# Kernel optimization log

Hardware: AMD Instinct MI355X
Metric: run time of the kernel (lower is better)

## Reference

```python
import jax, jax.numpy as jnp
import numpy as np

D_MODEL = 1024
EXPAND = 2
D_INNER = D_MODEL * EXPAND  # 2048
D_STATE = 16
FFN_HIDDEN = ((D_MODEL * 4 * 2 // 3) + 63) // 64 * 64  # 2752
EPS = 1e-6


def rmsnorm(x, w):
    return x * jax.lax.rsqrt(jnp.mean(x * x, axis=-1, keepdims=True) + EPS) * w


def selective_scan(z, dt_w, dt_b, x_proj_w, A_log, Dp):
    # z: [B, L, d_inner]
    dt = jax.nn.softplus(jnp.einsum('bld,ed->ble', z, dt_w) + dt_b)     # [B,L,d]
    BC = jnp.einsum('bld,nd->bln', z, x_proj_w)                          # [B,L,2n]
    Bm, Cm = BC[..., :D_STATE], BC[..., D_STATE:]                        # [B,L,n]
    A = -jnp.exp(A_log)                                                  # [d,n]
    dA = jnp.exp(dt[..., None] * A)                                      # [B,L,d,n]
    dBz = (dt * z)[..., None] * Bm[:, :, None, :]                        # [B,L,d,n]

    def combine(e1, e2):
        a1, b1 = e1
        a2, b2 = e2
        return (a1 * a2, a2 * b1 + b2)

    _, h = jax.lax.associative_scan(combine, (dA, dBz), axis=1)          # [B,L,d,n]
    y = jnp.einsum('bldn,bln->bld', h, Cm) + z * Dp
    return y


def setup_inputs() -> dict:
    key = jax.random.key(0)
    ks = jax.random.split(key, 12)
    s = 0.02
    inp = {
        'x': jax.random.normal(ks[0], (2, 1024, D_MODEL), dtype=jnp.float32),
        'norm1_w': jnp.ones((D_MODEL,), jnp.float32),
        'in_proj_w': jax.random.normal(ks[1], (D_INNER, D_MODEL), jnp.float32) * s,
        'gate_proj_w': jax.random.normal(ks[2], (D_INNER, D_MODEL), jnp.float32) * s,
        'dt_w': jax.random.normal(ks[3], (D_INNER, D_INNER), jnp.float32) * s,
        'dt_b': jnp.full((D_INNER,), -2.0, jnp.float32),
        'x_proj_w': jax.random.normal(ks[4], (2 * D_STATE, D_INNER), jnp.float32) * s,
        'A_log': jnp.broadcast_to(jnp.log(jnp.arange(1, D_STATE + 1, dtype=jnp.float32)), (D_INNER, D_STATE)).copy(),
        'Dp': jnp.ones((D_INNER,), jnp.float32),
        'out_proj_w': jax.random.normal(ks[5], (D_MODEL, D_INNER), jnp.float32) * s,
        'ffn_norm_w': jnp.ones((D_MODEL,), jnp.float32),
        'ffn_gate_w': jax.random.normal(ks[6], (FFN_HIDDEN, D_MODEL), jnp.float32) * s,
        'ffn_up_w': jax.random.normal(ks[7], (FFN_HIDDEN, D_MODEL), jnp.float32) * s,
        'ffn_down_w': jax.random.normal(ks[8], (D_MODEL, FFN_HIDDEN), jnp.float32) * s,
    }
    return inp


def reference(x, norm1_w, in_proj_w, gate_proj_w, dt_w, dt_b, x_proj_w, A_log, Dp,
              out_proj_w, ffn_norm_w, ffn_gate_w, ffn_up_w, ffn_down_w):
    residual = x
    h = rmsnorm(x, norm1_w)
    z = jnp.einsum('bld,ed->ble', h, in_proj_w)
    gate = jax.nn.sigmoid(jnp.einsum('bld,ed->ble', h, gate_proj_w))
    z = z * gate
    ssm_out = selective_scan(z, dt_w, dt_b, x_proj_w, A_log, Dp)
    x = residual + jnp.einsum('ble,de->bld', ssm_out, out_proj_w)
    hn = rmsnorm(x, ffn_norm_w)
    ff = jnp.einsum('blh,dh->bld',
                    jax.nn.silu(jnp.einsum('bld,hd->blh', hn, ffn_gate_w)) *
                    jnp.einsum('bld,hd->blh', hn, ffn_up_w),
                    ffn_down_w)
    return x + ff
```

## Files before the change

### kernel.cpp

```cpp
#include <hip/hip_runtime.h>
#include <cstdint>
#include <cstddef>


#define BM 128
#define BN 128
#define BK 32

typedef __attribute__((ext_vector_type(8))) short short8;
typedef __attribute__((ext_vector_type(4))) float floatx4;

__device__ __forceinline__ unsigned short f2bf(float f) {
  unsigned int u = __builtin_bit_cast(unsigned int, f);
  u = u + 0x7fffu + ((u >> 16) & 1u);
  return (unsigned short)(u >> 16);
}

__device__ __forceinline__ void async_copy16(const unsigned short* g, unsigned short* l) {
  __builtin_amdgcn_global_load_lds(
      (__attribute__((address_space(1))) void*)(const_cast<unsigned short*>(g)),
      (__attribute__((address_space(3))) void*)(l), 16, 0, 0);
}

struct Seg { const float* src; unsigned short* dst; int mode; int aux; };
struct CvtArgs { Seg sg[10]; int g0[11]; };

__global__ __launch_bounds__(256) void cvt_all(
    CvtArgs a, int nCvt,
    const float* __restrict__ x, const float* __restrict__ nw,
    unsigned short* __restrict__ h_bf) {
  __shared__ float ws_[4];
  if ((int)blockIdx.x >= nCvt) {
    int row = blockIdx.x - nCvt, t = threadIdx.x;
    float4 v = *(const float4*)&x[(size_t)row * 1024 + t * 4];
    float ss = v.x * v.x + v.y * v.y + v.z * v.z + v.w * v.w;
#pragma unroll
    for (int m = 1; m < 64; m <<= 1) ss += __shfl_xor(ss, m);
    if ((t & 63) == 0) ws_[t >> 6] = ss;
    __syncthreads();
    float tot = ws_[0] + ws_[1] + ws_[2] + ws_[3];
    float scale = rsqrtf(tot * (1.0f / 1024.0f) + 1e-6f);
    ushort4 o;
    o.x = f2bf(v.x * scale * nw[t * 4 + 0]);
    o.y = f2bf(v.y * scale * nw[t * 4 + 1]);
    o.z = f2bf(v.z * scale * nw[t * 4 + 2]);
    o.w = f2bf(v.w * scale * nw[t * 4 + 3]);
    *(ushort4*)&h_bf[(size_t)row * 1024 + t * 4] = o;
    return;
  }
  int i = blockIdx.x * 256 + threadIdx.x;
  if (i >= a.g0[10]) return;
  int s = 0;
#pragma unroll
  for (int k = 1; k < 10; ++k) s += (i >= a.g0[k]) ? 1 : 0;
  int li = i - a.g0[s];
  Seg sg = a.sg[s];
  if (sg.mode == 2) {
    ushort4 z = {0, 0, 0, 0};
    *(ushort4*)&sg.dst[(size_t)li * 4] = z;
  } else if (sg.mode == 0) {
    float4 v = *(const float4*)&sg.src[(size_t)li * 4];
    ushort4 o = {f2bf(v.x), f2bf(v.y), f2bf(v.z), f2bf(v.w)};
    *(ushort4*)&sg.dst[(size_t)li * 4] = o;
  } else {
    int r = li >> 8, c = li & 255;
    float4 v = *(const float4*)&sg.src[(size_t)li * 4];
    ushort4 o = {f2bf(v.x), f2bf(v.y), f2bf(v.z), f2bf(v.w)};
    *(ushort4*)&sg.dst[((size_t)(2 * r + sg.aux) * 256 + c) * 4] = o;
  }
}

__global__ __launch_bounds__(256) void rmsnorm_fuse3(
    const float* __restrict__ x, const float* __restrict__ p,
    const float* __restrict__ w,
    float* __restrict__ x2, unsigned short* __restrict__ outbf) {
  int row = blockIdx.x, t = threadIdx.x;
  size_t off = (size_t)row * 1024 + t * 4;
  float4 a = *(const float4*)&x[off];
  float4 b = *(const float4*)&p[off];
  float4 c = *(const float4*)&p[2097152ull + off];
  float4 d = *(const float4*)&p[4194304ull + off];
  float4 e = *(const float4*)&p[6291456ull + off];
  float4 v = {a.x + b.x + c.x + d.x + e.x, a.y + b.y + c.y + d.y + e.y,
              a.z + b.z + c.z + d.z + e.z, a.w + b.w + c.w + d.w + e.w};
  *(float4*)&x2[off] = v;
  float ss = v.x * v.x + v.y * v.y + v.z * v.z + v.w * v.w;
#pragma unroll
  for (int m = 1; m < 64; m <<= 1) ss += __shfl_xor(ss, m);
  __shared__ float ws_[4];
  if ((t & 63) == 0) ws_[t >> 6] = ss;
  __syncthreads();
  float tot = ws_[0] + ws_[1] + ws_[2] + ws_[3];
  float scale = rsqrtf(tot * (1.0f / 1024.0f) + 1e-6f);
  ushort4 o;
  o.x = f2bf(v.x * scale * w[t * 4 + 0]);
  o.y = f2bf(v.y * scale * w[t * 4 + 1]);
  o.z = f2bf(v.z * scale * w[t * 4 + 2]);
  o.w = f2bf(v.w * scale * w[t * 4 + 3]);
  *(ushort4*)&outbf[off] = o;
}

__global__ void final_add(const float* __restrict__ x2, const float* __restrict__ p,
                          float* __restrict__ out) {
  int i = blockIdx.x * 256 + threadIdx.x;
  float4 a = ((const float4*)x2)[i];
  float4 b = ((const float4*)p)[i];
  float4 c = ((const float4*)(p + 2097152ull))[i];
  float4 d = ((const float4*)(p + 4194304ull))[i];
  float4 e = ((const float4*)(p + 6291456ull))[i];
  float4 o = {a.x + b.x + c.x + d.x + e.x, a.y + b.y + c.y + d.y + e.y,
              a.z + b.z + c.z + d.z + e.z, a.w + b.w + c.w + d.w + e.w};
  ((float4*)out)[i] = o;
}

template <int EPI, int MAP>
__global__ __launch_bounds__(256, 4) void gemm_bt(
    const unsigned short* __restrict__ A,
    const unsigned short* __restrict__ W1,
    const unsigned short* __restrict__ W2,
    int n1_blocks, int ncols, int K,
    void* __restrict__ Cv, int ldc,
    float* __restrict__ C2) {
  __shared__ __align__(16) unsigned short As[2][BM * BK];
  __shared__ __align__(16) unsigned short Bs[2][BN * BK];
  int bn, bm, ks = 0, k0 = 0, nk;
  if (MAP == 0) {
    bn = blockIdx.x; bm = blockIdx.y;
    nk = K / BK;
  } else if (MAP == 2) {
    int l = blockIdx.x, i = l >> 3;
    bn = (l & 7) + 8 * (i % 6);
    bm = i / 6;
    if (bn >= ncols) return;
    nk = K / BK;
  } else if (MAP == 3) {
    bn = blockIdx.x & 7; bm = blockIdx.y;
    ks = blockIdx.x >> 3;
    int nkt = K / BK, base = nkt >> 2, rem = nkt & 3;
    nk = base + (ks < rem ? 1 : 0);
    int k0t = ks * base + (ks < rem ? ks : rem);
    k0 = k0t * BK;
  } else {
    if ((int)blockIdx.y < gridDim.y - 1) { bn = blockIdx.x; bm = blockIdx.y; }
    else                                 { bn = n1_blocks;  bm = blockIdx.x; }
    ks = blockIdx.z;
    k0 = ks * (K >> 1);
    nk = (K >> 1) / BK;
  }
  const int tid = threadIdx.x;
  const int wave = tid >> 6, lane = tid & 63;
  const unsigned short* W;
  int wrow0;
  if (bn < n1_blocks) { W = W1; wrow0 = bn * BN; }
  else                { W = W2; wrow0 = (bn - n1_blocks) * BN; }
  const int m0 = bm * BM;
  const int wm = wave >> 1, wn = wave & 1;
  const int l15 = lane & 15, quad = lane >> 4;

  floatx4 acc[4][4] = {};

  const int c0 = wave * 64 + lane;
  const int r0 = c0 >> 2, k0off = ((c0 & 3) ^ ((r0 >> 1) & 3)) * 8;
  const int c1 = c0 + 256;
  const int r1 = c1 >> 2, k1off = ((c1 & 3) ^ ((r1 >> 1) & 3)) * 8;

  auto stage = [&](int kb, int buf) {
    async_copy16(A + (size_t)(m0 + r0) * K + kb + k0off, &As[buf][c0 * 8]);
    async_copy16(A + (size_t)(m0 + r1) * K + kb + k1off, &As[buf][c1 * 8]);
    async_copy16(W + (size_t)(wrow0 + r0) * K + kb + k0off, &Bs[buf][c0 * 8]);
    async_copy16(W + (size_t)(wrow0 + r1) * K + kb + k1off, &Bs[buf][c1 * 8]);
  };

  stage(k0, 0);
  for (int kt = 0; kt < nk; ++kt) {
    const int cur = kt & 1;
    __syncthreads();
    if (kt + 1 < nk) stage(k0 + (kt + 1) * BK, cur ^ 1);

    short8 af[4], bf4[4];
#pragma unroll
    for (int i = 0; i < 4; ++i) {
      int row = wm * 64 + i * 16 + l15;
      af[i] = *(const short8*)&As[cur][(row * 4 + (quad ^ ((row >> 1) & 3))) * 8];
    }
#pragma unroll
    for (int j = 0; j < 4; ++j) {
      int row = wn * 64 + j * 16 + l15;
      bf4[j] = *(const short8*)&Bs[cur][(row * 4 + (quad ^ ((row >> 1) & 3))) * 8];
    }
#pragma unroll
    for (int i = 0; i < 4; ++i)
#pragma unroll
      for (int j = 0; j < 4; ++j)
        acc[i][j] = __builtin_amdgcn_mfma_f32_16x16x32_bf16(af[i], bf4[j], acc[i][j], 0, 0, 0);
  }

#pragma unroll
  for (int i = 0; i < 4; ++i)
#pragma unroll
    for (int j = 0; j < 4; ++j)
#pragma unroll
      for (int r = 0; r < 4; ++r) {
        int gr = m0 + wm * 64 + i * 16 + quad * 4 + r;
        int lc = wn * 64 + j * 16 + l15;
        int gc = bn * BN + lc;
        float v = acc[i][j][r];
        if (EPI == 3) {
          ((float*)Cv)[(size_t)ks * 2097152 + (size_t)gr * ldc + gc] = v;
        } else if (EPI == 4) {
          if (bn < n1_blocks)
            ((float*)Cv)[(size_t)ks * 4194304 + (size_t)gr * ldc + gc] = v;
          else
            C2[(size_t)ks * 262144 + (size_t)gr * 128 + lc] = v;
        } else if (EPI == 5) {
          float other = __shfl_xor(v, 1);
          if (!(l15 & 1)) {
            float zv = v / (1.0f + __expf(-other));
            int f = gc >> 1;
            ((float*)Cv)[(size_t)gr * 2048 + f] = zv;
            ((unsigned short*)C2)[(size_t)gr * 2048 + f] = f2bf(zv);
          }
        } else {
          float other = __shfl_xor(v, 1);
          if (!(l15 & 1)) {
            int f = gc >> 1;
            if (f < 2752) {
              float av = v / (1.0f + __expf(-v)) * other;
              ((unsigned short*)Cv)[(size_t)gr * 2752 + f] = f2bf(av);
            }
          }
        }
      }
}

__device__ __forceinline__ void stage_bc2(const float* __restrict__ pb,
                                          int b, int c, float* bcs, int tid) {
  int row = tid >> 3, c4 = tid & 7;
  size_t idx = ((size_t)b * 1024 + c * 32 + row) * 128 + c4 * 4;
  float4 aa = *(const float4*)&pb[idx];
  float4 bb = *(const float4*)&pb[262144ull + idx];
  float4 sm = {aa.x + bb.x, aa.y + bb.y, aa.z + bb.z, aa.w + bb.w};
  *(float4*)&bcs[row * 32 + c4 * 4] = sm;
}

__device__ __forceinline__ float softplus_f(float v) {
  return fmaxf(v, 0.0f) + log1pf(__expf(-fabsf(v)));
}

__global__ __launch_bounds__(256) void scan_phase1(
    const float* __restrict__ pd, const float* __restrict__ pb,
    const float* __restrict__ dtb, const float* __restrict__ z,
    const float* __restrict__ A_log,
    float* __restrict__ P, float* __restrict__ S) {
  const int d = blockIdx.x * 256 + threadIdx.x;
  const int c = blockIdx.y, b = blockIdx.z;
  __shared__ float bcs[1024];
  stage_bc2(pb, b, c, bcs, threadIdx.x);
  __syncthreads();
  float A2[16];
#pragma unroll
  for (int n = 0; n < 16; ++n) A2[n] = -__expf(A_log[d * 16 + n]) * 1.44269504f;
  const float bias = dtb[d];
  float p[16], s[16];
#pragma unroll
  for (int n = 0; n < 16; ++n) { p[n] = 1.0f; s[n] = 0.0f; }
  const size_t base = ((size_t)b * 1024 + c * 32) * 2048 + d;
#pragma unroll 4
  for (int t = 0; t < 32; ++t) {
    size_t off = base + (size_t)t * 2048;
    float dtv = softplus_f(pd[off] + pd[4194304ull + off] + bias);
    float zv  = z[off];
    float dtz = dtv * zv;
#pragma unroll
    for (int n = 0; n < 16; ++n) {
      float dA = exp2f(dtv * A2[n]);
      s[n] = __builtin_fmaf(dA, s[n], dtz * bcs[t * 32 + n]);
      p[n] *= dA;
    }
  }
  float* Pp = P + (((size_t)c * 2 + b) * 2048 + d) * 16;
  float* Sp = S + (((size_t)c * 2 + b) * 2048 + d) * 16;
#pragma unroll
  for (int n = 0; n < 16; ++n) { Pp[n] = p[n]; Sp[n] = s[n]; }
}

__global__ __launch_bounds__(256) void scan_phase2(
    const float* __restrict__ P, const float* __restrict__ S,
    float* __restrict__ H) {
  int i = blockIdx.x * 256 + threadIdx.x;
  float h = 0.0f;
#pragma unroll
  for (int c = 0; c < 32; ++c) {
    size_t idx = (size_t)c * 65536 + i;
    H[idx] = h;
    h = __builtin_fmaf(P[idx], h, S[idx]);
  }
}

__global__ __launch_bounds__(256) void scan_phase3(
    const float* __restrict__ pd, const float* __restrict__ pb,
    const float* __restrict__ dtb, const float* __restrict__ z,
    const float* __restrict__ A_log, const float* __restrict__ Dp,
    const float* __restrict__ H, unsigned short* __restrict__ ybf) {
  const int d = blockIdx.x * 256 + threadIdx.x;
  const int c = blockIdx.y, b = blockIdx.z;
  __shared__ float bcs[1024];
  stage_bc2(pb, b, c, bcs, threadIdx.x);
  __syncthreads();
  float A2[16];
#pragma unroll
  for (int n = 0; n < 16; ++n) A2[n] = -__expf(A_log[d * 16 + n]) * 1.44269504f;
  const float bias = dtb[d];
  float h[16];
  const float* Hp = H + (((size_t)c * 2 + b) * 2048 + d) * 16;
#pragma unroll
  for (int n = 0; n < 16; ++n) h[n] = Hp[n];
  const float Dd = Dp[d];
  const size_t base = ((size_t)b * 1024 + c * 32) * 2048 + d;
#pragma unroll 4
  for (int t = 0; t < 32; ++t) {
    size_t off = base + (size_t)t * 2048;
    float dtv = softplus_f(pd[off] + pd[4194304ull + off] + bias);
    float zv  = z[off];
    float dtz = dtv * zv;
    float y = zv * Dd;
#pragma unroll
    for (int n = 0; n < 16; ++n) {
      float dA = exp2f(dtv * A2[n]);
      h[n] = __builtin_fmaf(dA, h[n], dtz * bcs[t * 32 + n]);
      y = __builtin_fmaf(h[n], bcs[t * 32 + 16 + n], y);
    }
    ybf[off] = f2bf(y);
  }
}

extern "C" void kernel_launch(void* const* d_in, const int* in_sizes, int n_in,
                              void* d_out, int out_size, void* d_ws, size_t ws_size,
                              hipStream_t stream) {
  const float* x         = (const float*)d_in[0];
  const float* norm1_w   = (const float*)d_in[1];
  const float* in_proj_w = (const float*)d_in[2];
  const float* gate_w    = (const float*)d_in[3];
  const float* dt_w      = (const float*)d_in[4];
  const float* dt_b      = (const float*)d_in[5];
  const float* x_proj_w  = (const float*)d_in[6];
  const float* A_log     = (const float*)d_in[7];
  const float* Dp        = (const float*)d_in[8];
  const float* out_w     = (const float*)d_in[9];
  const float* ffn_nw    = (const float*)d_in[10];
  const float* ffn_g     = (const float*)d_in[11];
  const float* ffn_u     = (const float*)d_in[12];
  const float* ffn_d     = (const float*)d_in[13];
  float* out = (float*)d_out;

  char* p = (char*)d_ws;
  auto alloc = [&](size_t b) { char* r = p; p += (b + 255) & ~(size_t)255; return r; };
  unsigned short* h_bf   = (unsigned short*)alloc(2048ull * 1024 * 2);
  float* big             = (float*)alloc(2048ull * 5632 * 4);
  float* pk              = (float*)alloc(4ull * 2048 * 1024 * 4);
  float* pkb             = (float*)alloc(2ull * 2048 * 128 * 4);
  float* z32             = (float*)alloc(2048ull * 2048 * 4);
  unsigned short* zbf    = (unsigned short*)alloc(2048ull * 2048 * 2);
  unsigned short* ybf    = (unsigned short*)alloc(2048ull * 2048 * 2);
  float* x2              = (float*)alloc(2048ull * 1024 * 4);
  unsigned short* hn_bf  = (unsigned short*)alloc(2048ull * 1024 * 2);
  unsigned short* act_bf = (unsigned short*)alloc(2048ull * 2752 * 2);
  unsigned short* w_zg   = (unsigned short*)alloc(4096ull * 1024 * 2);
  unsigned short* w_dt   = (unsigned short*)alloc(2048ull * 2048 * 2);
  unsigned short* w_xp   = (unsigned short*)alloc(128ull * 2048 * 2);
  unsigned short* w_out  = (unsigned short*)alloc(1024ull * 2048 * 2);
  unsigned short* w_gu   = (unsigned short*)alloc(5632ull * 1024 * 2);
  unsigned short* w_d    = (unsigned short*)alloc(1024ull * 2752 * 2);

  float* pkd = big;
  float* Pb = pk;
  float* Sb = pk + 2097152;
  float* Hb = pk + 4194304;

  CvtArgs ca;
  auto seg = [&](int idx, const float* s, unsigned short* d, int mode, int aux, int groups,
                 int& acc_g) {
    ca.sg[idx] = {s, d, mode, aux};
    ca.g0[idx] = acc_g;
    acc_g += groups;
  };
  int acc_g = 0;
  seg(0, in_proj_w, w_zg,                 1, 0, 2048 * 256, acc_g);
  seg(1, gate_w,    w_zg,                 1, 1, 2048 * 256, acc_g);
  seg(2, dt_w,      w_dt,                 0, 0, 2048 * 512, acc_g);
  seg(3, x_proj_w,  w_xp,                 0, 0, 32 * 512,   acc_g);
  seg(4, nullptr,   w_xp + 32ull * 2048,  2, 0, 96 * 512,   acc_g);
  seg(5, out_w,     w_out,                0, 0, 1024 * 512, acc_g);
  seg(6, ffn_g,     w_gu,                 1, 0, 2752 * 256, acc_g);
  seg(7, ffn_u,     w_gu,                 1, 1, 2752 * 256, acc_g);
  seg(8, nullptr,   w_gu + 5504ull * 1024, 2, 0, 128 * 256, acc_g);
  seg(9, ffn_d,     w_d,                  0, 0, 1024 * 688, acc_g);
  ca.g0[10] = acc_g;
  int nCvt = (acc_g + 255) / 256;
  cvt_all<<<nCvt + 2048, 256, 0, stream>>>(ca, nCvt, x, norm1_w, h_bf);

  gemm_bt<5, 0><<<dim3(32, 16), 256, 0, stream>>>(h_bf, w_zg, w_zg, 32, 0, 1024, z32, 2048, (float*)zbf);
  gemm_bt<4, 4><<<dim3(16, 17, 2), 256, 0, stream>>>(zbf, w_dt, w_xp, 16, 0, 2048, pkd, 2048, pkb);
  scan_phase1<<<dim3(8, 32, 2), 256, 0, stream>>>(pkd, pkb, dt_b, z32, A_log, Pb, Sb);
  scan_phase2<<<256, 256, 0, stream>>>(Pb, Sb, Hb);
  scan_phase3<<<dim3(8, 32, 2), 256, 0, stream>>>(pkd, pkb, dt_b, z32, A_log, Dp, Hb, ybf);
  gemm_bt<3, 3><<<dim3(32, 16), 256, 0, stream>>>(ybf, w_out, w_out, 8, 0, 2048, pk, 1024, nullptr);
  rmsnorm_fuse3<<<2048, 256, 0, stream>>>(x, pk, ffn_nw, x2, hn_bf);
  gemm_bt<6, 2><<<768, 256, 0, stream>>>(hn_bf, w_gu, w_gu, 44, 44, 1024, act_bf, 2752, nullptr);
  gemm_bt<3, 3><<<dim3(32, 16), 256, 0, stream>>>(act_bf, w_d, w_d, 8, 0, 2752, pk, 1024, nullptr);
  final_add<<<2048, 256, 0, stream>>>(x2, pk, out);
}
```

Before: 400.7 us.

## Halve scan chunk length and cache softplus dt between scan phases

The chunked selective scan now uses 64 chunks of 16 timesteps instead of 32 chunks of 32, doubling the number of blocks in phases 1 and 3 so more of the GPU is occupied. Phase 1 also writes the softplus dt values to a new fp32 buffer, and phase 3 reads them back instead of reloading two split-K partials and recomputing softplus. Phase 2's sequential pass becomes twice as long, P/S/H storage doubles (H moves into the big buffer), and the extra dt write/read adds memory traffic.

```diff
diff --git a/kernel.cpp b/kernel.cpp
--- a/kernel.cpp
+++ b/kernel.cpp
@@ -233,14 +233,19 @@
       }
 }
 
+#define NCH 64
+#define CHL 16
+
 __device__ __forceinline__ void stage_bc2(const float* __restrict__ pb,
                                           int b, int c, float* bcs, int tid) {
-  int row = tid >> 3, c4 = tid & 7;
-  size_t idx = ((size_t)b * 1024 + c * 32 + row) * 128 + c4 * 4;
-  float4 aa = *(const float4*)&pb[idx];
-  float4 bb = *(const float4*)&pb[262144ull + idx];
-  float4 sm = {aa.x + bb.x, aa.y + bb.y, aa.z + bb.z, aa.w + bb.w};
-  *(float4*)&bcs[row * 32 + c4 * 4] = sm;
+  if (tid < 128) {
+    int row = tid >> 3, c4 = tid & 7;
+    size_t idx = ((size_t)b * 1024 + c * CHL + row) * 128 + c4 * 4;
+    float4 aa = *(const float4*)&pb[idx];
+    float4 bb = *(const float4*)&pb[262144ull + idx];
+    float4 sm = {aa.x + bb.x, aa.y + bb.y, aa.z + bb.z, aa.w + bb.w};
+    *(float4*)&bcs[row * 32 + c4 * 4] = sm;
+  }
 }
 
 __device__ __forceinline__ float softplus_f(float v) {
@@ -250,11 +255,11 @@
 __global__ __launch_bounds__(256) void scan_phase1(
     const float* __restrict__ pd, const float* __restrict__ pb,
     const float* __restrict__ dtb, const float* __restrict__ z,
-    const float* __restrict__ A_log,
+    const float* __restrict__ A_log, float* __restrict__ dt32,
     float* __restrict__ P, float* __restrict__ S) {
   const int d = blockIdx.x * 256 + threadIdx.x;
   const int c = blockIdx.y, b = blockIdx.z;
-  __shared__ float bcs[1024];
+  __shared__ float bcs[CHL * 32];
   stage_bc2(pb, b, c, bcs, threadIdx.x);
   __syncthreads();
   float A2[16];
@@ -264,11 +269,12 @@
   float p[16], s[16];
 #pragma unroll
   for (int n = 0; n < 16; ++n) { p[n] = 1.0f; s[n] = 0.0f; }
-  const size_t base = ((size_t)b * 1024 + c * 32) * 2048 + d;
+  const size_t base = ((size_t)b * 1024 + c * CHL) * 2048 + d;
 #pragma unroll 4
-  for (int t = 0; t < 32; ++t) {
+  for (int t = 0; t < CHL; ++t) {
     size_t off = base + (size_t)t * 2048;
     float dtv = softplus_f(pd[off] + pd[4194304ull + off] + bias);
+    dt32[off] = dtv;
     float zv  = z[off];
     float dtz = dtv * zv;
 #pragma unroll
@@ -290,7 +296,7 @@
   int i = blockIdx.x * 256 + threadIdx.x;
   float h = 0.0f;
 #pragma unroll
-  for (int c = 0; c < 32; ++c) {
+  for (int c = 0; c < NCH; ++c) {
     size_t idx = (size_t)c * 65536 + i;
     H[idx] = h;
     h = __builtin_fmaf(P[idx], h, S[idx]);
@@ -298,29 +304,28 @@
 }
 
 __global__ __launch_bounds__(256) void scan_phase3(
-    const float* __restrict__ pd, const float* __restrict__ pb,
-    const float* __restrict__ dtb, const float* __restrict__ z,
-    const float* __restrict__ A_log, const float* __restrict__ Dp,
-    const float* __restrict__ H, unsigned short* __restrict__ ybf) {
+    const float* __restrict__ dt32, const float* __restrict__ pb,
+    const float* __restrict__ z, const float* __restrict__ A_log,
+    const float* __restrict__ Dp, const float* __restrict__ H,
+    unsigned short* __restrict__ ybf) {
   const int d = blockIdx.x * 256 + threadIdx.x;
   const int c = blockIdx.y, b = blockIdx.z;
-  __shared__ float bcs[1024];
+  __shared__ float bcs[CHL * 32];
   stage_bc2(pb, b, c, bcs, threadIdx.x);
   __syncthreads();
   float A2[16];
 #pragma unroll
   for (int n = 0; n < 16; ++n) A2[n] = -__expf(A_log[d * 16 + n]) * 1.44269504f;
-  const float bias = dtb[d];
   float h[16];
   const float* Hp = H + (((size_t)c * 2 + b) * 2048 + d) * 16;
 #pragma unroll
   for (int n = 0; n < 16; ++n) h[n] = Hp[n];
   const float Dd = Dp[d];
-  const size_t base = ((size_t)b * 1024 + c * 32) * 2048 + d;
+  const size_t base = ((size_t)b * 1024 + c * CHL) * 2048 + d;
 #pragma unroll 4
-  for (int t = 0; t < 32; ++t) {
+  for (int t = 0; t < CHL; ++t) {
     size_t off = base + (size_t)t * 2048;
-    float dtv = softplus_f(pd[off] + pd[4194304ull + off] + bias);
+    float dtv = dt32[off];
     float zv  = z[off];
     float dtz = dtv * zv;
     float y = zv * Dd;
@@ -361,6 +366,7 @@
   float* pkb             = (float*)alloc(2ull * 2048 * 128 * 4);
   float* z32             = (float*)alloc(2048ull * 2048 * 4);
   unsigned short* zbf    = (unsigned short*)alloc(2048ull * 2048 * 2);
+  float* dt32            = (float*)alloc(2048ull * 2048 * 4);
   unsigned short* ybf    = (unsigned short*)alloc(2048ull * 2048 * 2);
   float* x2              = (float*)alloc(2048ull * 1024 * 4);
   unsigned short* hn_bf  = (unsigned short*)alloc(2048ull * 1024 * 2);
@@ -373,9 +379,9 @@
   unsigned short* w_d    = (unsigned short*)alloc(1024ull * 2752 * 2);
 
   float* pkd = big;
-  float* Pb = pk;
-  float* Sb = pk + 2097152;
-  float* Hb = pk + 4194304;
+  float* Hb  = big;
+  float* Pb  = pk;
+  float* Sb  = pk + 4194304;
 
   CvtArgs ca;
   auto seg = [&](int idx, const float* s, unsigned short* d, int mode, int aux, int groups,
@@ -401,9 +407,9 @@
 
   gemm_bt<5, 0><<<dim3(32, 16), 256, 0, stream>>>(h_bf, w_zg, w_zg, 32, 0, 1024, z32, 2048, (float*)zbf);
   gemm_bt<4, 4><<<dim3(16, 17, 2), 256, 0, stream>>>(zbf, w_dt, w_xp, 16, 0, 2048, pkd, 2048, pkb);
-  scan_phase1<<<dim3(8, 32, 2), 256, 0, stream>>>(pkd, pkb, dt_b, z32, A_log, Pb, Sb);
+  scan_phase1<<<dim3(8, NCH, 2), 256, 0, stream>>>(pkd, pkb, dt_b, z32, A_log, dt32, Pb, Sb);
   scan_phase2<<<256, 256, 0, stream>>>(Pb, Sb, Hb);
-  scan_phase3<<<dim3(8, 32, 2), 256, 0, stream>>>(pkd, pkb, dt_b, z32, A_log, Dp, Hb, ybf);
+  scan_phase3<<<dim3(8, NCH, 2), 256, 0, stream>>>(dt32, pkb, z32, A_log, Dp, Hb, ybf);
   gemm_bt<3, 3><<<dim3(32, 16), 256, 0, stream>>>(ybf, w_out, w_out, 8, 0, 2048, pk, 1024, nullptr);
   rmsnorm_fuse3<<<2048, 256, 0, stream>>>(x, pk, ffn_nw, x2, hn_bf);
   gemm_bt<6, 2><<<768, 256, 0, stream>>>(hn_bf, w_gu, w_gu, 44, 44, 1024, act_bf, 2752, nullptr);
```

Measured after the change: 385.8 us. 1.04x faster.
